# Kernel optimization log

Hardware: AMD Instinct MI355X
Metric: run time of the kernel (lower is better)

The kernel has to match this reference:

```python
import jax, jax.numpy as jnp
import numpy as np

HIDDEN = 1024
NUM_HEADS = 16
HEAD_DIM = HIDDEN // NUM_HEADS
GRID_SIZE = 5
SPLINE_ORDER = 3
NUM_COEF = GRID_SIZE + SPLINE_ORDER  # 8


def make_grid(in_features):
    # efficient-kan default grid: range [-1, 1], extended by spline_order on each side
    h = 2.0 / GRID_SIZE
    g = jnp.arange(-SPLINE_ORDER, GRID_SIZE + SPLINE_ORDER + 1, dtype=jnp.float32) * h - 1.0
    return jnp.broadcast_to(g, (in_features, g.shape[0]))  # (in, G+2k+1)


def b_splines(x, grid):
    # x: (N, in); grid: (in, G+2k+1) -> bases (N, in, G+k)
    x = x[..., None]
    bases = ((x >= grid[:, :-1]) & (x < grid[:, 1:])).astype(x.dtype)
    for k in range(1, SPLINE_ORDER + 1):
        left = (x - grid[:, : -(k + 1)]) / (grid[:, k:-1] - grid[:, : -(k + 1)])
        right = (grid[:, k + 1 :] - x) / (grid[:, k + 1 :] - grid[:, 1:-k])
        bases = left * bases[..., :-1] + right * bases[..., 1:]
    return bases


def kan_linear(x, base_w, spline_w, spline_scaler):
    # x: (..., in); base_w: (out, in); spline_w: (out, in, C); spline_scaler: (out, in)
    in_f = x.shape[-1]
    x2 = x.reshape(-1, in_f)
    base = jax.nn.silu(x2) @ base_w.T
    bases = b_splines(x2, make_grid(in_f))                      # (N, in, C)
    sw = spline_w * spline_scaler[..., None]                    # (out, in, C)
    spline = bases.reshape(x2.shape[0], -1) @ sw.reshape(sw.shape[0], -1).T
    return (base + spline).reshape(*x.shape[:-1], base_w.shape[0])


def apply_rope(x):
    # x: (B, H, S, D); interleaved rotary (lucidrains convention), theta=10000
    d, s = x.shape[-1], x.shape[-2]
    inv_freq = 1.0 / (10000.0 ** (jnp.arange(0, d, 2, dtype=jnp.float32) / d))
    freqs = jnp.arange(s, dtype=jnp.float32)[:, None] * inv_freq[None, :]  # (S, d/2)
    cos = jnp.repeat(jnp.cos(freqs), 2, axis=-1)
    sin = jnp.repeat(jnp.sin(freqs), 2, axis=-1)
    x1, x2 = x[..., 0::2], x[..., 1::2]
    rot = jnp.stack((-x2, x1), axis=-1).reshape(x.shape)
    return x * cos + rot * sin


def setup_inputs() -> dict:
    key = jax.random.key(0)
    ks = jax.random.split(key, 10)
    B, S, H = 2, 2048, HIDDEN
    H3 = 3 * H
    scale = 0.02
    return {
        "q": jax.random.normal(ks[0], (B, S, H), jnp.float32),
        "k": jax.random.normal(ks[1], (B, S, H), jnp.float32),
        "v": jax.random.normal(ks[2], (B, S, H), jnp.float32),
        "attn_mask": jnp.zeros((S, S), jnp.float32),
        "qkv_base_w": jax.random.normal(ks[3], (H3, H3), jnp.float32) * scale,
        "qkv_spline_w": jax.random.normal(ks[4], (H3, H3, NUM_COEF), jnp.float32) * scale,
        "qkv_scaler": jnp.ones((H3, H3), jnp.float32),
        "out_base_w": jax.random.normal(ks[5], (H, H), jnp.float32) * scale,
        "out_spline_w": jax.random.normal(ks[6], (H, H, NUM_COEF), jnp.float32) * scale,
        "out_scaler": jnp.ones((H, H), jnp.float32),
    }


def reference(q, k, v, attn_mask, qkv_base_w, qkv_spline_w, qkv_scaler,
              out_base_w, out_spline_w, out_scaler):
    B, S, H = q.shape
    x = jnp.concatenate((q, k, v), axis=2)                       # (B, S, 3H)
    qkv = kan_linear(x, qkv_base_w, qkv_spline_w, qkv_scaler)    # (B, S, 3H)
    qkv = qkv.reshape(B, S, NUM_HEADS, 3 * HEAD_DIM).transpose(0, 2, 1, 3)
    queries, keys, values = jnp.split(qkv, 3, axis=-1)           # each (B, nh, S, hd)
    queries = apply_rope(queries)
    keys = apply_rope(keys)
    scores = jnp.einsum("bhqd,bhkd->bhqk", queries, keys) / (HEAD_DIM ** 0.5) + attn_mask
    attention = jax.nn.softmax(scores, axis=-1)
    context = jnp.einsum("bhqk,bhkd->bhqd", attention, values)
    context = context.transpose(0, 2, 1, 3).reshape(B, S, H)
    return kan_linear(context, out_base_w, out_spline_w, out_scaler)
```

## Files before the change

### kernel.cpp

```cpp
#include <hip/hip_runtime.h>
#include <hip/hip_bf16.h>
#include <stdint.h>

typedef __bf16 bf16;
typedef __attribute__((ext_vector_type(8))) __bf16 bf16x8;
typedef __attribute__((ext_vector_type(4))) float f32x4;

#define DEVI __device__ __forceinline__

constexpr int BATCH = 2, SEQ = 2048, HID = 1024, NHEAD = 16, HDIM = 64;
constexpr int H3 = 3072;
constexpr int MROWS = BATCH * SEQ;
constexpr int KEXP = 9;
constexpr int K1DIM = H3 * KEXP;
constexpr int K2DIM = HID * KEXP;

constexpr size_t WQ_OFF  = 0;
constexpr size_t AQ_OFF  = 169869312;
constexpr size_t CQ_OFF  = AQ_OFF + 226492416;
constexpr size_t QR_OFF  = CQ_OFF + 50331648;
constexpr size_t KR_OFF  = QR_OFF + 8388608;
constexpr size_t VB_OFF  = KR_OFF + 8388608;
constexpr size_t CTX_OFF = VB_OFF + 8388608;
constexpr size_t A2_OFF  = 0;
constexpr size_t W2_OFF  = 75497472;

DEVI void gld_lds16(const void* g, void* l) {
  __builtin_amdgcn_global_load_lds((const __attribute__((address_space(1))) void*)g,
                                   (__attribute__((address_space(3))) void*)l, 16, 0, 0);
}

DEVI void silu_bases(float x, float* o9) {
  o9[0] = x / (1.0f + __expf(-x));
  float g[12];
#pragma unroll
  for (int j = 0; j < 12; ++j) g[j] = (float)(j - 3) * 0.4f - 1.0f;
  float b[11];
#pragma unroll
  for (int j = 0; j < 11; ++j) b[j] = (x >= g[j] && x < g[j + 1]) ? 1.0f : 0.0f;
#pragma unroll
  for (int k = 1; k <= 3; ++k) {
    const float inv = (k == 1) ? 2.5f : (k == 2) ? 1.25f : (1.0f / 1.2f);
#pragma unroll
    for (int j = 0; j + k < 11; ++j) {
      b[j] = (x - g[j]) * inv * b[j] + (g[j + k + 1] - x) * inv * b[j + 1];
    }
  }
#pragma unroll
  for (int c = 0; c < 8; ++c) o9[1 + c] = b[c];
}

__global__ __launch_bounds__(256)
void wprep_kernel(const float* __restrict__ bw, const float* __restrict__ sw,
                  const float* __restrict__ sc, bf16* __restrict__ W, int KK) {
  __shared__ bf16 buf[256 * KEXP];
  const int tid = threadIdx.x;
  const int n = blockIdx.y;
  const int i0 = blockIdx.x * 256;
  const size_t idx = (size_t)n * KK + i0 + tid;
  float base = bw[idx];
  float scal = sc[idx];
  const float4* sp = (const float4*)(sw + idx * 8);
  float4 s0 = sp[0], s1 = sp[1];
  bf16* o = buf + tid * KEXP;
  o[0] = (bf16)base;
  o[1] = (bf16)(s0.x * scal); o[2] = (bf16)(s0.y * scal);
  o[3] = (bf16)(s0.z * scal); o[4] = (bf16)(s0.w * scal);
  o[5] = (bf16)(s1.x * scal); o[6] = (bf16)(s1.y * scal);
  o[7] = (bf16)(s1.z * scal); o[8] = (bf16)(s1.w * scal);
  __syncthreads();
  bf16* dst = W + (size_t)n * KK * KEXP + (size_t)i0 * KEXP;
#pragma unroll
  for (int j = tid; j < 256 * KEXP / 8; j += 256)
    *(bf16x8*)(dst + j * 8) = *(const bf16x8*)(buf + j * 8);
}

__global__ __launch_bounds__(256)
void act_qkv_kernel(const float* __restrict__ qin, const float* __restrict__ kin,
                    const float* __restrict__ vin, bf16* __restrict__ A) {
  __shared__ bf16 buf[256 * KEXP];
  const int tid = threadIdx.x;
  const int m = blockIdx.y;
  const int i0 = blockIdx.x * 256;
  const int i = i0 + tid;
  const int which = i >> 10, off = i & 1023;
  const float* src = (which == 0) ? qin : (which == 1) ? kin : vin;
  float x = src[(size_t)m * HID + off];
  float o9[9];
  silu_bases(x, o9);
  bf16* o = buf + tid * KEXP;
#pragma unroll
  for (int c = 0; c < 9; ++c) o[c] = (bf16)o9[c];
  __syncthreads();
  bf16* dst = A + (size_t)m * K1DIM + (size_t)i0 * KEXP;
#pragma unroll
  for (int j = tid; j < 256 * KEXP / 8; j += 256)
    *(bf16x8*)(dst + j * 8) = *(const bf16x8*)(buf + j * 8);
}

__global__ __launch_bounds__(256)
void act_out_kernel(const float* __restrict__ ctx, bf16* __restrict__ A) {
  __shared__ bf16 buf[256 * KEXP];
  const int tid = threadIdx.x;
  const int m = blockIdx.y;
  const int i0 = blockIdx.x * 256;
  float x = ctx[(size_t)m * HID + i0 + tid];
  float o9[9];
  silu_bases(x, o9);
  bf16* o = buf + tid * KEXP;
#pragma unroll
  for (int c = 0; c < 9; ++c) o[c] = (bf16)o9[c];
  __syncthreads();
  bf16* dst = A + (size_t)m * K2DIM + (size_t)i0 * KEXP;
#pragma unroll
  for (int j = tid; j < 256 * KEXP / 8; j += 256)
    *(bf16x8*)(dst + j * 8) = *(const bf16x8*)(buf + j * 8);
}

__global__ __launch_bounds__(256, 4)
void gemm_kernel(const bf16* __restrict__ A, const bf16* __restrict__ Bw,
                 float* __restrict__ C, int N, int K) {
  __shared__ bf16 As[128 * 64];
  __shared__ bf16 Bs[128 * 64];
  const int tid = threadIdx.x;
  const int lane = tid & 63;
  const int l15 = lane & 15, lq = lane >> 4;
  const int wid = tid >> 6;
  const int wm = (wid >> 1) * 64, wn = (wid & 1) * 64;
  const int gx = gridDim.x;
  const int nwg = gx * gridDim.y;
  const int orig = blockIdx.y * gx + blockIdx.x;
  const int swz = (orig & 7) * (nwg >> 3) + (orig >> 3);
  const int bm = swz / gx;
  const int bn = swz % gx;
  f32x4 acc[4][4] = {};
  const int srow = tid >> 3;
  const int schk = (tid & 7) ^ (srow & 7);
  const bf16* aB = A + (size_t)(bm * 128 + srow) * K + schk * 8;
  const bf16* bB = Bw + (size_t)(bn * 128 + srow) * K + schk * 8;

  int aoff[2][4], boff[2][4];
#pragma unroll
  for (int ks = 0; ks < 2; ++ks) {
#pragma unroll
    for (int f = 0; f < 4; ++f) {
      int arow = wm + f * 16 + l15;
      int brow = wn + f * 16 + l15;
      aoff[ks][f] = arow * 64 + (((ks * 4 + lq) ^ (arow & 7)) * 8);
      boff[ks][f] = brow * 64 + (((ks * 4 + lq) ^ (brow & 7)) * 8);
    }
  }

  for (int kt = 0; kt < K; kt += 64) {
#pragma unroll
    for (int r = 0; r < 4; ++r) {
      gld_lds16(aB + (size_t)(r * 32) * K + kt, As + r * 2048 + tid * 8);
      gld_lds16(bB + (size_t)(r * 32) * K + kt, Bs + r * 2048 + tid * 8);
    }
    __syncthreads();
#pragma unroll
    for (int ks = 0; ks < 2; ++ks) {
      bf16x8 af[4], bfr[4];
#pragma unroll
      for (int mf = 0; mf < 4; ++mf)
        af[mf] = *(const bf16x8*)&As[aoff[ks][mf]];
#pragma unroll
      for (int nf = 0; nf < 4; ++nf)
        bfr[nf] = *(const bf16x8*)&Bs[boff[ks][nf]];
#pragma unroll
      for (int mf = 0; mf < 4; ++mf)
#pragma unroll
        for (int nf = 0; nf < 4; ++nf)
          acc[mf][nf] = __builtin_amdgcn_mfma_f32_16x16x32_bf16(af[mf], bfr[nf], acc[mf][nf], 0, 0, 0);
    }
    __syncthreads();
  }
#pragma unroll
  for (int mf = 0; mf < 4; ++mf)
#pragma unroll
    for (int nf = 0; nf < 4; ++nf)
#pragma unroll
      for (int r = 0; r < 4; ++r) {
        int row = bm * 128 + wm + mf * 16 + lq * 4 + r;
        int col = bn * 128 + wn + nf * 16 + l15;
        C[(size_t)row * N + col] = acc[mf][nf][r];
      }
}

__global__ void rope_kernel(const float* __restrict__ Cq, bf16* __restrict__ qr,
                            bf16* __restrict__ kr, bf16* __restrict__ vb) {
  int idx = blockIdx.x * blockDim.x + threadIdx.x;
  int p = idx & 31;
  int h = (idx >> 5) & 15;
  int m = idx >> 9;
  int s = m & (SEQ - 1);
  int b = m >> 11;
  const float* row = Cq + (size_t)m * H3 + h * 192;
  float q0 = row[2 * p], q1 = row[2 * p + 1];
  float k0 = row[64 + 2 * p], k1 = row[64 + 2 * p + 1];
  float v0 = row[128 + 2 * p], v1 = row[128 + 2 * p + 1];
  float invf = expf(-(float)p * (9.210340371976184f / 32.0f));
  float fr = (float)s * invf;
  float sn, cs;
  sincosf(fr, &sn, &cs);
  size_t o = (((size_t)(b * NHEAD + h)) * SEQ + s) * 64 + 2 * p;
  qr[o] = (bf16)(q0 * cs - q1 * sn); qr[o + 1] = (bf16)(q1 * cs + q0 * sn);
  kr[o] = (bf16)(k0 * cs - k1 * sn); kr[o + 1] = (bf16)(k1 * cs + k0 * sn);
  vb[o] = (bf16)v0; vb[o + 1] = (bf16)v1;
}

__global__ __launch_bounds__(256, 2)
void attn_kernel(const bf16* __restrict__ qr, const bf16* __restrict__ kr,
                 const bf16* __restrict__ vb, const float* __restrict__ mask,
                 float* __restrict__ ctx) {
  __shared__ bf16 Kt[64 * 64];
  __shared__ bf16 Vt[64 * 64];
  __shared__ bf16 Pl[4][16 * 64];
  const int tid = threadIdx.x, lane = tid & 63, wid = tid >> 6;
  const int l15 = lane & 15, lq = lane >> 4;
  const int qt = blockIdx.x, bh = blockIdx.y;
  const int b = bh >> 4, hh = bh & 15;
  const size_t baseQ = ((size_t)bh * SEQ + qt * 64 + wid * 16) * 64;
  bf16x8 aq[2];
  aq[0] = *(const bf16x8*)&qr[baseQ + (size_t)l15 * 64 + 0 + lq * 8];
  aq[1] = *(const bf16x8*)&qr[baseQ + (size_t)l15 * 64 + 32 + lq * 8];
  float mrow[4], lrow[4];
  f32x4 oacc[4] = {};
#pragma unroll
  for (int r = 0; r < 4; ++r) { mrow[r] = -1e30f; lrow[r] = 0.0f; }
  const float scale = 0.125f;
  for (int kv0 = 0; kv0 < SEQ; kv0 += 64) {
    const bf16* kBase = kr + ((size_t)bh * SEQ + kv0 + (tid >> 3)) * 64 + (tid & 7) * 8;
#pragma unroll
    for (int r = 0; r < 2; ++r)
      gld_lds16(kBase + (size_t)(r * 32) * 64, Kt + r * 2048 + tid * 8);
#pragma unroll
    for (int r = 0; r < 2; ++r) {
      int row = r * 32 + (tid >> 3);
      int c8 = (tid & 7) * 8;
      bf16x8 vv = *(const bf16x8*)&vb[((size_t)bh * SEQ + kv0 + row) * 64 + c8];
#pragma unroll
      for (int e = 0; e < 8; ++e) Vt[(c8 + e) * 64 + row] = vv[e];
    }
    __syncthreads();
    f32x4 sacc[4] = {};
#pragma unroll
    for (int k0 = 0; k0 < 2; ++k0) {
#pragma unroll
      for (int nf = 0; nf < 4; ++nf) {
        bf16x8 bk = *(const bf16x8*)&Kt[(nf * 16 + l15) * 64 + k0 * 32 + lq * 8];
        sacc[nf] = __builtin_amdgcn_mfma_f32_16x16x32_bf16(aq[k0], bk, sacc[nf], 0, 0, 0);
      }
    }
    const int qg0 = qt * 64 + wid * 16 + lq * 4;
#pragma unroll
    for (int nf = 0; nf < 4; ++nf) {
      int kvg = kv0 + nf * 16 + l15;
#pragma unroll
      for (int r = 0; r < 4; ++r)
        sacc[nf][r] = sacc[nf][r] * scale + mask[(size_t)(qg0 + r) * SEQ + kvg];
    }
    float fac[4];
#pragma unroll
    for (int r = 0; r < 4; ++r) {
      float v = fmaxf(fmaxf(sacc[0][r], sacc[1][r]), fmaxf(sacc[2][r], sacc[3][r]));
      v = fmaxf(v, __shfl_xor(v, 1));
      v = fmaxf(v, __shfl_xor(v, 2));
      v = fmaxf(v, __shfl_xor(v, 4));
      v = fmaxf(v, __shfl_xor(v, 8));
      float mnew = fmaxf(mrow[r], v);
      fac[r] = __expf(mrow[r] - mnew);
      mrow[r] = mnew;
    }
    float rs[4] = {0, 0, 0, 0};
#pragma unroll
    for (int nf = 0; nf < 4; ++nf)
#pragma unroll
      for (int r = 0; r < 4; ++r) {
        float pv = __expf(sacc[nf][r] - mrow[r]);
        sacc[nf][r] = pv;
        rs[r] += pv;
      }
#pragma unroll
    for (int r = 0; r < 4; ++r) {
      float v = rs[r];
      v += __shfl_xor(v, 1); v += __shfl_xor(v, 2);
      v += __shfl_xor(v, 4); v += __shfl_xor(v, 8);
      lrow[r] = lrow[r] * fac[r] + v;
    }
#pragma unroll
    for (int nf = 0; nf < 4; ++nf)
#pragma unroll
      for (int r = 0; r < 4; ++r)
        Pl[wid][(lq * 4 + r) * 64 + nf * 16 + l15] = (bf16)sacc[nf][r];
#pragma unroll
    for (int nf = 0; nf < 4; ++nf)
#pragma unroll
      for (int r = 0; r < 4; ++r)
        oacc[nf][r] *= fac[r];
#pragma unroll
    for (int k0 = 0; k0 < 2; ++k0) {
      bf16x8 ap = *(const bf16x8*)&Pl[wid][l15 * 64 + k0 * 32 + lq * 8];
#pragma unroll
      for (int nf = 0; nf < 4; ++nf) {
        bf16x8 bv = *(const bf16x8*)&Vt[(nf * 16 + l15) * 64 + k0 * 32 + lq * 8];
        oacc[nf] = __builtin_amdgcn_mfma_f32_16x16x32_bf16(ap, bv, oacc[nf], 0, 0, 0);
      }
    }
    __syncthreads();
  }
#pragma unroll
  for (int nf = 0; nf < 4; ++nf)
#pragma unroll
    for (int r = 0; r < 4; ++r) {
      int row = qt * 64 + wid * 16 + lq * 4 + r;
      int col = hh * 64 + nf * 16 + l15;
      ctx[((size_t)b * SEQ + row) * HID + col] = oacc[nf][r] / lrow[r];
    }
}

extern "C" void kernel_launch(void* const* d_in, const int* in_sizes, int n_in,
                              void* d_out, int out_size, void* d_ws, size_t ws_size,
                              hipStream_t stream) {
  const float* qin    = (const float*)d_in[0];
  const float* kin    = (const float*)d_in[1];
  const float* vin    = (const float*)d_in[2];
  const float* mask   = (const float*)d_in[3];
  const float* qkv_bw = (const float*)d_in[4];
  const float* qkv_sw = (const float*)d_in[5];
  const float* qkv_sc = (const float*)d_in[6];
  const float* out_bw = (const float*)d_in[7];
  const float* out_sw = (const float*)d_in[8];
  const float* out_sc = (const float*)d_in[9];
  char* ws = (char*)d_ws;
  bf16* Wq  = (bf16*)(ws + WQ_OFF);
  bf16* Aq  = (bf16*)(ws + AQ_OFF);
  float* Cq = (float*)(ws + CQ_OFF);
  bf16* qr  = (bf16*)(ws + QR_OFF);
  bf16* kr  = (bf16*)(ws + KR_OFF);
  bf16* vb  = (bf16*)(ws + VB_OFF);
  float* ctx = (float*)(ws + CTX_OFF);
  bf16* A2  = (bf16*)(ws + A2_OFF);
  bf16* W2  = (bf16*)(ws + W2_OFF);

  wprep_kernel<<<dim3(H3 / 256, H3), 256, 0, stream>>>(qkv_bw, qkv_sw, qkv_sc, Wq, H3);
  act_qkv_kernel<<<dim3(H3 / 256, MROWS), 256, 0, stream>>>(qin, kin, vin, Aq);
  gemm_kernel<<<dim3(H3 / 128, MROWS / 128), 256, 0, stream>>>(Aq, Wq, Cq, H3, K1DIM);
  rope_kernel<<<(MROWS * NHEAD * 32) / 256, 256, 0, stream>>>(Cq, qr, kr, vb);
  attn_kernel<<<dim3(SEQ / 64, BATCH * NHEAD), 256, 0, stream>>>(qr, kr, vb, mask, ctx);
  act_out_kernel<<<dim3(HID / 256, MROWS), 256, 0, stream>>>(ctx, A2);
  wprep_kernel<<<dim3(HID / 256, HID), 256, 0, stream>>>(out_bw, out_sw, out_sc, W2, HID);
  gemm_kernel<<<dim3(HID / 128, MROWS / 128), 256, 0, stream>>>(A2, W2, (float*)d_out, HID, K2DIM);
}
```

Measured before the change: 1.247 ms.

## Double-buffer GEMM LDS tiles and XOR-swizzle attention K/V/P shared memory

```diff
diff --git a/kernel.cpp b/kernel.cpp
--- a/kernel.cpp
+++ b/kernel.cpp
@@ -29,6 +29,10 @@
   __builtin_amdgcn_global_load_lds((const __attribute__((address_space(1))) void*)g,
                                    (__attribute__((address_space(3))) void*)l, 16, 0, 0);
 }
+
+#define WAITVM0() asm volatile("s_waitcnt vmcnt(0)" ::: "memory")
+#define MEMFENCE() asm volatile("" ::: "memory")
+#define BARRIER() do { __builtin_amdgcn_s_barrier(); asm volatile("" ::: "memory"); } while (0)
 
 DEVI void silu_bases(float x, float* o9) {
   o9[0] = x / (1.0f + __expf(-x));
@@ -117,22 +121,17 @@
     *(bf16x8*)(dst + j * 8) = *(const bf16x8*)(buf + j * 8);
 }
 
-__global__ __launch_bounds__(256, 4)
+__global__ __launch_bounds__(256, 2)
 void gemm_kernel(const bf16* __restrict__ A, const bf16* __restrict__ Bw,
                  float* __restrict__ C, int N, int K) {
-  __shared__ bf16 As[128 * 64];
-  __shared__ bf16 Bs[128 * 64];
+  __shared__ bf16 As[2][128 * 64];
+  __shared__ bf16 Bs[2][128 * 64];
   const int tid = threadIdx.x;
   const int lane = tid & 63;
   const int l15 = lane & 15, lq = lane >> 4;
   const int wid = tid >> 6;
   const int wm = (wid >> 1) * 64, wn = (wid & 1) * 64;
-  const int gx = gridDim.x;
-  const int nwg = gx * gridDim.y;
-  const int orig = blockIdx.y * gx + blockIdx.x;
-  const int swz = (orig & 7) * (nwg >> 3) + (orig >> 3);
-  const int bm = swz / gx;
-  const int bn = swz % gx;
+  const int bm = blockIdx.y, bn = blockIdx.x;
   f32x4 acc[4][4] = {};
   const int srow = tid >> 3;
   const int schk = (tid & 7) ^ (srow & 7);
@@ -151,30 +150,45 @@
     }
   }
 
-  for (int kt = 0; kt < K; kt += 64) {
-#pragma unroll
-    for (int r = 0; r < 4; ++r) {
-      gld_lds16(aB + (size_t)(r * 32) * K + kt, As + r * 2048 + tid * 8);
-      gld_lds16(bB + (size_t)(r * 32) * K + kt, Bs + r * 2048 + tid * 8);
-    }
-    __syncthreads();
+#define GSTAGE(b_, kt_)                                                      \
+  do {                                                                       \
+    bf16* dA_ = &As[b_][0];                                                  \
+    bf16* dB_ = &Bs[b_][0];                                                  \
+    _Pragma("unroll")                                                        \
+    for (int r = 0; r < 4; ++r) {                                            \
+      gld_lds16(aB + (size_t)(r * 32) * K + (kt_), dA_ + r * 2048 + tid * 8);\
+      gld_lds16(bB + (size_t)(r * 32) * K + (kt_), dB_ + r * 2048 + tid * 8);\
+    }                                                                        \
+  } while (0)
+
+  const int nt = K >> 6;
+  GSTAGE(0, 0);
+  WAITVM0();
+  BARRIER();
+  for (int t = 0; t < nt; ++t) {
+    if (t + 1 < nt) { GSTAGE((t + 1) & 1, (size_t)(t + 1) * 64); MEMFENCE(); }
+    const bf16* as = &As[t & 1][0];
+    const bf16* bs = &Bs[t & 1][0];
 #pragma unroll
     for (int ks = 0; ks < 2; ++ks) {
       bf16x8 af[4], bfr[4];
 #pragma unroll
       for (int mf = 0; mf < 4; ++mf)
-        af[mf] = *(const bf16x8*)&As[aoff[ks][mf]];
+        af[mf] = *(const bf16x8*)(as + aoff[ks][mf]);
 #pragma unroll
       for (int nf = 0; nf < 4; ++nf)
-        bfr[nf] = *(const bf16x8*)&Bs[boff[ks][nf]];
+        bfr[nf] = *(const bf16x8*)(bs + boff[ks][nf]);
 #pragma unroll
       for (int mf = 0; mf < 4; ++mf)
 #pragma unroll
         for (int nf = 0; nf < 4; ++nf)
           acc[mf][nf] = __builtin_amdgcn_mfma_f32_16x16x32_bf16(af[mf], bfr[nf], acc[mf][nf], 0, 0, 0);
     }
-    __syncthreads();
+    WAITVM0();
+    BARRIER();
   }
+#undef GSTAGE
+
 #pragma unroll
   for (int mf = 0; mf < 4; ++mf)
 #pragma unroll
@@ -229,8 +243,10 @@
 #pragma unroll
   for (int r = 0; r < 4; ++r) { mrow[r] = -1e30f; lrow[r] = 0.0f; }
   const float scale = 0.125f;
+  const int krow = tid >> 3;
+  const int kchk = (tid & 7) ^ (krow & 7);
   for (int kv0 = 0; kv0 < SEQ; kv0 += 64) {
-    const bf16* kBase = kr + ((size_t)bh * SEQ + kv0 + (tid >> 3)) * 64 + (tid & 7) * 8;
+    const bf16* kBase = kr + ((size_t)bh * SEQ + kv0 + krow) * 64 + kchk * 8;
 #pragma unroll
     for (int r = 0; r < 2; ++r)
       gld_lds16(kBase + (size_t)(r * 32) * 64, Kt + r * 2048 + tid * 8);
@@ -240,7 +256,10 @@
       int c8 = (tid & 7) * 8;
       bf16x8 vv = *(const bf16x8*)&vb[((size_t)bh * SEQ + kv0 + row) * 64 + c8];
 #pragma unroll
-      for (int e = 0; e < 8; ++e) Vt[(c8 + e) * 64 + row] = vv[e];
+      for (int e = 0; e < 8; ++e) {
+        int d = c8 + e;
+        Vt[d * 64 + (((row >> 3) ^ (d & 7)) << 3) + (row & 7)] = vv[e];
+      }
     }
     __syncthreads();
     f32x4 sacc[4] = {};
@@ -248,7 +267,7 @@
     for (int k0 = 0; k0 < 2; ++k0) {
 #pragma unroll
       for (int nf = 0; nf < 4; ++nf) {
-        bf16x8 bk = *(const bf16x8*)&Kt[(nf * 16 + l15) * 64 + k0 * 32 + lq * 8];
+        bf16x8 bk = *(const bf16x8*)&Kt[(nf * 16 + l15) * 64 + (((k0 * 4 + lq) ^ (l15 & 7)) << 3)];
         sacc[nf] = __builtin_amdgcn_mfma_f32_16x16x32_bf16(aq[k0], bk, sacc[nf], 0, 0, 0);
       }
     }
@@ -291,8 +310,11 @@
 #pragma unroll
     for (int nf = 0; nf < 4; ++nf)
 #pragma unroll
-      for (int r = 0; r < 4; ++r)
-        Pl[wid][(lq * 4 + r) * 64 + nf * 16 + l15] = (bf16)sacc[nf][r];
+      for (int r = 0; r < 4; ++r) {
+        int qrow = lq * 4 + r;
+        int col = nf * 16 + l15;
+        Pl[wid][qrow * 64 + ((((col >> 3) ^ (qrow & 7))) << 3) + (col & 7)] = (bf16)sacc[nf][r];
+      }
 #pragma unroll
     for (int nf = 0; nf < 4; ++nf)
 #pragma unroll
@@ -300,10 +322,10 @@
         oacc[nf][r] *= fac[r];
 #pragma unroll
     for (int k0 = 0; k0 < 2; ++k0) {
-      bf16x8 ap = *(const bf16x8*)&Pl[wid][l15 * 64 + k0 * 32 + lq * 8];
+      bf16x8 ap = *(const bf16x8*)&Pl[wid][l15 * 64 + (((k0 * 4 + lq) ^ (l15 & 7)) << 3)];
 #pragma unroll
       for (int nf = 0; nf < 4; ++nf) {
-        bf16x8 bv = *(const bf16x8*)&Vt[(nf * 16 + l15) * 64 + k0 * 32 + lq * 8];
+        bf16x8 bv = *(const bf16x8*)&Vt[(nf * 16 + l15) * 64 + (((k0 * 4 + lq) ^ (l15 & 7)) << 3)];
         oacc[nf] = __builtin_amdgcn_mfma_f32_16x16x32_bf16(ap, bv, oacc[nf], 0, 0, 0);
       }
     }
```

Measured after the change: 1.582 ms. 26.9% more time.
